# Optimization experiments

Hardware: AMD Instinct MI355X
Metric: run time of the kernel (lower is better)

Reference implementation:

```python
import jax, jax.numpy as jnp
import numpy as np

B, S, D, H, W = 2, 2048, 1024, 16, 256
HD = D // H

def setup_inputs() -> dict:
    key = jax.random.key(0)
    k1, k2, k3 = jax.random.split(key, 3)
    x = jax.random.normal(k1, (B, S, D), dtype=jnp.float32)
    w_qkv = jax.random.normal(k2, (D, 3 * D), dtype=jnp.float32) * (D ** -0.5)
    b_qkv = jnp.zeros((3 * D,), dtype=jnp.float32)
    w_out = jax.random.normal(k3, (D, D), dtype=jnp.float32) * (D ** -0.5)
    b_out = jnp.zeros((D,), dtype=jnp.float32)
    return {"x": x, "w_qkv": w_qkv, "b_qkv": b_qkv, "w_out": w_out, "b_out": b_out}

def reference(x, w_qkv, b_qkv, w_out, b_out):
    b, s, d = x.shape
    qkv = x @ w_qkv + b_qkv                       # [B,S,3D]
    qkv = qkv.reshape(b, s, 3, H, HD)
    q = jnp.transpose(qkv[:, :, 0], (0, 2, 1, 3))  # [B,H,S,HD]
    k = jnp.transpose(qkv[:, :, 1], (0, 2, 1, 3))
    v = jnp.transpose(qkv[:, :, 2], (0, 2, 1, 3))
    # NOTE: original scales by d_model**0.5, not head_dim**0.5
    scores = jnp.einsum('bhqd,bhkd->bhqk', q, k) / (d ** 0.5)
    idx = jnp.arange(s)
    band = jnp.abs(idx[:, None] - idx[None, :]) <= W  # |i-j| <= window_size
    scores = jnp.where(band[None, None], scores, -jnp.inf)
    attn = jax.nn.softmax(scores, axis=-1)
    out = jnp.einsum('bhqk,bhkd->bhqd', attn, v)
    out = jnp.transpose(out, (0, 2, 1, 3)).reshape(b, s, d)
    return out @ w_out + b_out
```

## Files before the change

kernel.cpp:

```cpp
#include <hip/hip_runtime.h>
#include <cstdint>

typedef unsigned short u16;
typedef __attribute__((ext_vector_type(8))) short bf16x8;
typedef __attribute__((ext_vector_type(4))) float f32x4;
typedef __attribute__((ext_vector_type(8))) unsigned short u16x8;

#define DEV static __device__ __forceinline__

DEV u16 f2bf(float f) {
  union { float f; uint32_t u; } v; v.f = f;
  uint32_t r = (v.u + 0x7fffu + ((v.u >> 16) & 1u)) >> 16;
  return (u16)r;
}

DEV void async16(void* lds, const void* g) {
  __builtin_amdgcn_global_load_lds(
      (const __attribute__((address_space(1))) uint32_t*)g,
      (__attribute__((address_space(3))) uint32_t*)lds, 16, 0, 0);
}

__global__ void conv8(const float* __restrict__ in, u16* __restrict__ out, int n8) {
  int i = blockIdx.x * 256 + threadIdx.x;
  if (i >= n8) return;
  const float4* p = (const float4*)in + (size_t)i * 2;
  float4 a = p[0], b = p[1];
  u16x8 ov;
  ov[0] = f2bf(a.x); ov[1] = f2bf(a.y); ov[2] = f2bf(a.z); ov[3] = f2bf(a.w);
  ov[4] = f2bf(b.x); ov[5] = f2bf(b.y); ov[6] = f2bf(b.z); ov[7] = f2bf(b.w);
  *(u16x8*)(out + (size_t)i * 8) = ov;
}

__global__ void tconv(const float* __restrict__ in, u16* __restrict__ out, int R, int Cdim) {
  __shared__ float t[32][33];
  const int tx = threadIdx.x & 31, ty = threadIdx.x >> 5;
  const int r0 = blockIdx.y * 32, c0 = blockIdx.x * 32;
#pragma unroll
  for (int k = 0; k < 4; ++k) {
    int r = ty + k * 8;
    t[r][tx] = in[(size_t)(r0 + r) * Cdim + c0 + tx];
  }
  __syncthreads();
#pragma unroll
  for (int k = 0; k < 4; ++k) {
    int cc = ty + k * 8;
    out[(size_t)(c0 + cc) * R + r0 + tx] = f2bf(t[tx][cc]);
  }
}

template <int EPI>
__global__ __launch_bounds__(256, 2) void gemm_bt(
    const u16* __restrict__ A, const u16* __restrict__ BT,
    const float* __restrict__ bias, float* __restrict__ C,
    u16* __restrict__ qb, u16* __restrict__ kbuf, u16* __restrict__ vtb,
    int Mdim, int Ndim, int Kdim)
{
  __shared__ u16 Alds[128 * 64];
  __shared__ u16 Blds[128 * 64];
  const int tid = threadIdx.x;
  const int wid = tid >> 6, lane = tid & 63;
  const int g = lane >> 4, c = lane & 15;
  const int wr = wid >> 1, wc = wid & 1;
  const int row0 = blockIdx.y * 128, col0 = blockIdx.x * 128;

  f32x4 acc[4][4] = {};

  for (int kt = 0; kt < Kdim; kt += 64) {
    __syncthreads();
#pragma unroll
    for (int it = 0; it < 4; ++it) {
      int chunk = wid * 256 + it * 64 + lane;
      int r = chunk >> 3, j = chunk & 7;
      int js = j ^ (r & 7);
      async16((char*)Alds + (wid * 256 + it * 64) * 16,
              A + (size_t)(row0 + r) * Kdim + kt + js * 8);
      async16((char*)Blds + (wid * 256 + it * 64) * 16,
              BT + (size_t)(col0 + r) * Kdim + kt + js * 8);
    }
    __syncthreads();
#pragma unroll
    for (int kk = 0; kk < 2; ++kk) {
      bf16x8 av[4], bv[4];
#pragma unroll
      for (int mi = 0; mi < 4; ++mi) {
        int r = wr * 64 + mi * 16 + c;
        int js = (kk * 4 + g) ^ (r & 7);
        av[mi] = *(const bf16x8*)((const char*)Alds + r * 128 + js * 16);
      }
#pragma unroll
      for (int ni = 0; ni < 4; ++ni) {
        int r = wc * 64 + ni * 16 + c;
        int js = (kk * 4 + g) ^ (r & 7);
        bv[ni] = *(const bf16x8*)((const char*)Blds + r * 128 + js * 16);
      }
#pragma unroll
      for (int mi = 0; mi < 4; ++mi)
#pragma unroll
        for (int ni = 0; ni < 4; ++ni)
          acc[mi][ni] = __builtin_amdgcn_mfma_f32_16x16x32_bf16(
              av[mi], bv[ni], acc[mi][ni], 0, 0, 0);
    }
  }

#pragma unroll
  for (int mi = 0; mi < 4; ++mi) {
#pragma unroll
    for (int ni = 0; ni < 4; ++ni) {
      int colg = col0 + wc * 64 + ni * 16 + c;
      float bsv = bias[colg];
#pragma unroll
      for (int r = 0; r < 4; ++r) {
        int rowg = row0 + wr * 64 + mi * 16 + g * 4 + r;
        float val = acc[mi][ni][r] + bsv;
        if (EPI == 0) {
          C[(size_t)rowg * Ndim + colg] = val;
        } else {
          int t = colg >> 10, rem = colg & 1023;
          int h = rem >> 6, hd = rem & 63;
          int b = rowg >> 11, s = rowg & 2047;
          size_t bho = (size_t)(b * 16 + h);
          u16 bvv = f2bf(val);
          if (t == 0)      qb  [(bho * 2048 + s) * 64 + hd] = bvv;
          else if (t == 1) kbuf[(bho * 2048 + s) * 64 + hd] = bvv;
          else             vtb [(bho * 64 + hd) * 2048 + s] = bvv;
        }
      }
    }
  }
}

__global__ __launch_bounds__(256, 2) void attn_win(
    const u16* __restrict__ qb, const u16* __restrict__ kb,
    const u16* __restrict__ vtb, u16* __restrict__ hb)
{
  constexpr int S = 2048, W = 256;
  __shared__ u16 Klds[64 * 64];
  __shared__ u16 Vlds[64 * 64];
  __shared__ u16 Plds[4][16 * 64];

  const int tid = threadIdx.x, wid = tid >> 6, lane = tid & 63;
  const int g = lane >> 4, c = lane & 15;
  const int bh = blockIdx.y, qt = blockIdx.x;
  const int q0 = qt * 64;
  const size_t bho = (size_t)bh * S * 64;

  bf16x8 aq[2];
  {
    const u16* qrow = qb + bho + (size_t)(q0 + wid * 16 + c) * 64;
    aq[0] = *(const bf16x8*)(qrow + g * 8);
    aq[1] = *(const bf16x8*)(qrow + 32 + g * 8);
  }
  f32x4 o[4] = {};
  float m[4] = {-1e30f, -1e30f, -1e30f, -1e30f};
  float lsum[4] = {0.f, 0.f, 0.f, 0.f};

  const int kstart = (q0 - W > 0) ? (q0 - W) : 0;
  const int kend = (q0 + 64 + W < S) ? (q0 + 64 + W) : S;
  const float rscale = 0.03125f;

  for (int k0 = kstart; k0 < kend; k0 += 64) {
    __syncthreads();
#pragma unroll
    for (int it = 0; it < 2; ++it) {
      int chunk = wid * 128 + it * 64 + lane;
      int r = chunk >> 3, j = chunk & 7;
      int js = j ^ (r & 7);
      async16((char*)Klds + (wid * 128 + it * 64) * 16,
              kb + bho + (size_t)(k0 + r) * 64 + js * 8);
      async16((char*)Vlds + (wid * 128 + it * 64) * 16,
              vtb + bho + (size_t)r * S + k0 + js * 8);
    }
    __syncthreads();

    f32x4 sacc[4] = {};
#pragma unroll
    for (int kb4 = 0; kb4 < 4; ++kb4) {
      int krow = kb4 * 16 + c;
#pragma unroll
      for (int kk = 0; kk < 2; ++kk) {
        int js = (kk * 4 + g) ^ (krow & 7);
        bf16x8 bk = *(const bf16x8*)((const char*)Klds + krow * 128 + js * 16);
        sacc[kb4] = __builtin_amdgcn_mfma_f32_16x16x32_bf16(aq[kk], bk, sacc[kb4], 0, 0, 0);
      }
    }

    const int qrb = q0 + wid * 16 + g * 4;
    float sc[4][4];
#pragma unroll
    for (int kb4 = 0; kb4 < 4; ++kb4) {
      int key = k0 + kb4 * 16 + c;
#pragma unroll
      for (int r = 0; r < 4; ++r) {
        int d = qrb + r - key;
        bool valid = (d <= W) && (d >= -W);
        sc[kb4][r] = valid ? sacc[kb4][r] * rscale : -1e30f;
      }
    }
    float fscale[4];
#pragma unroll
    for (int r = 0; r < 4; ++r) {
      float mx = fmaxf(fmaxf(sc[0][r], sc[1][r]), fmaxf(sc[2][r], sc[3][r]));
      mx = fmaxf(mx, __shfl_xor(mx, 1));
      mx = fmaxf(mx, __shfl_xor(mx, 2));
      mx = fmaxf(mx, __shfl_xor(mx, 4));
      mx = fmaxf(mx, __shfl_xor(mx, 8));
      float mnew = fmaxf(m[r], mx);
      fscale[r] = __expf(m[r] - mnew);
      m[r] = mnew;
    }
    float rowsum[4] = {0.f, 0.f, 0.f, 0.f};
    u16* Pw = &Plds[wid][0];
#pragma unroll
    for (int kb4 = 0; kb4 < 4; ++kb4) {
#pragma unroll
      for (int r = 0; r < 4; ++r) {
        float p = (sc[kb4][r] > -1e29f) ? __expf(sc[kb4][r] - m[r]) : 0.0f;
        rowsum[r] += p;
        int row = g * 4 + r;
        int key = kb4 * 16 + c;
        int jsw = (key >> 3) ^ (row & 7);
        *((u16*)((char*)Pw + row * 128 + jsw * 16 + (key & 7) * 2)) = f2bf(p);
      }
    }
#pragma unroll
    for (int r = 0; r < 4; ++r) {
      float s2 = rowsum[r];
      s2 += __shfl_xor(s2, 1);
      s2 += __shfl_xor(s2, 2);
      s2 += __shfl_xor(s2, 4);
      s2 += __shfl_xor(s2, 8);
      lsum[r] = lsum[r] * fscale[r] + s2;
      o[0][r] *= fscale[r]; o[1][r] *= fscale[r];
      o[2][r] *= fscale[r]; o[3][r] *= fscale[r];
    }
    asm volatile("s_waitcnt lgkmcnt(0)" ::: "memory");
#pragma unroll
    for (int ks = 0; ks < 2; ++ks) {
      int js = (ks * 4 + g) ^ (c & 7);
      bf16x8 pa = *(const bf16x8*)((const char*)Pw + c * 128 + js * 16);
#pragma unroll
      for (int nb = 0; nb < 4; ++nb) {
        int hd = nb * 16 + c;
        int vjs = (ks * 4 + g) ^ (hd & 7);
        bf16x8 bv = *(const bf16x8*)((const char*)Vlds + hd * 128 + vjs * 16);
        o[nb] = __builtin_amdgcn_mfma_f32_16x16x32_bf16(pa, bv, o[nb], 0, 0, 0);
      }
    }
  }

  const int b = bh >> 4, h = bh & 15;
#pragma unroll
  for (int nb = 0; nb < 4; ++nb) {
#pragma unroll
    for (int r = 0; r < 4; ++r) {
      int qr = q0 + wid * 16 + g * 4 + r;
      int col = h * 64 + nb * 16 + c;
      float val = o[nb][r] / lsum[r];
      hb[(size_t)(b * 2048 + qr) * 1024 + col] = f2bf(val);
    }
  }
}

extern "C" void kernel_launch(void* const* d_in, const int* in_sizes, int n_in,
                              void* d_out, int out_size, void* d_ws, size_t ws_size,
                              hipStream_t stream) {
  const float* x     = (const float*)d_in[0];
  const float* w_qkv = (const float*)d_in[1];
  const float* b_qkv = (const float*)d_in[2];
  const float* w_out = (const float*)d_in[3];
  const float* b_out = (const float*)d_in[4];
  float* out = (float*)d_out;

  char* ws = (char*)d_ws;
  const size_t MB = 1024 * 1024;
  u16* xbf   = (u16*)(ws);
  u16* wqT   = (u16*)(ws + 8 * MB);
  u16* woT   = (u16*)(ws + 14 * MB);
  u16* qbuf  = (u16*)(ws + 16 * MB);
  u16* kbuf  = (u16*)(ws + 24 * MB);
  u16* vtbuf = (u16*)(ws + 32 * MB);
  u16* hbuf  = (u16*)(ws + 40 * MB);

  conv8<<<dim3(4096 * 1024 / 8 / 256), 256, 0, stream>>>(x, xbf, 4096 * 1024 / 8);
  tconv<<<dim3(3072 / 32, 1024 / 32), 256, 0, stream>>>(w_qkv, wqT, 1024, 3072);
  tconv<<<dim3(1024 / 32, 1024 / 32), 256, 0, stream>>>(w_out, woT, 1024, 1024);
  gemm_bt<1><<<dim3(3072 / 128, 4096 / 128), 256, 0, stream>>>(
      xbf, wqT, b_qkv, nullptr, qbuf, kbuf, vtbuf, 4096, 3072, 1024);
  attn_win<<<dim3(2048 / 64, 32), 256, 0, stream>>>(qbuf, kbuf, vtbuf, hbuf);
  gemm_bt<0><<<dim3(1024 / 128, 4096 / 128), 256, 0, stream>>>(
      hbuf, woT, b_out, out, nullptr, nullptr, nullptr, 4096, 1024, 1024);
}
```

Baseline: 179.5 us.

## Restructure windowed attention with double-buffered K/V, larger tiles, lazy rescale

The attention kernel now processes 128 queries per 512-thread block and double-buffers K/V tiles in LDS so the next tile loads while the current one is computed. It skips waves whose rows lie entirely outside the band, skips masking on fully in-band tiles, and folds log2(e) into the scale so it can use exp2. The running max is only rescaled when it grows by more than a threshold. Both GEMM and attention block indices are remapped in an XCD-aware order to improve cache locality. This adds complexity and more LDS per block, and the lazy rescale can change numerics slightly.

```diff
diff --git a/kernel.cpp b/kernel.cpp
--- a/kernel.cpp
+++ b/kernel.cpp
@@ -1,5 +1,6 @@
 #include <hip/hip_runtime.h>
 #include <cstdint>
+#include <cmath>
 
 typedef unsigned short u16;
 typedef __attribute__((ext_vector_type(8))) short bf16x8;
@@ -13,6 +14,8 @@
   uint32_t r = (v.u + 0x7fffu + ((v.u >> 16) & 1u)) >> 16;
   return (u16)r;
 }
+
+DEV float fexp2(float x) { return exp2f(x); }
 
 DEV void async16(void* lds, const void* g) {
   __builtin_amdgcn_global_load_lds(
@@ -61,7 +64,11 @@
   const int wid = tid >> 6, lane = tid & 63;
   const int g = lane >> 4, c = lane & 15;
   const int wr = wid >> 1, wc = wid & 1;
-  const int row0 = blockIdx.y * 128, col0 = blockIdx.x * 128;
+  const int gx = gridDim.x;
+  const int nwg = gx * gridDim.y;
+  const int lin = blockIdx.y * gx + blockIdx.x;
+  const int work = (lin & 7) * (nwg >> 3) + (lin >> 3);
+  const int row0 = (work / gx) * 128, col0 = (work % gx) * 128;
 
   f32x4 acc[4][4] = {};
 
@@ -129,24 +136,27 @@
   }
 }
 
-__global__ __launch_bounds__(256, 2) void attn_win(
+__global__ __launch_bounds__(512, 4) void attn_win(
     const u16* __restrict__ qb, const u16* __restrict__ kb,
     const u16* __restrict__ vtb, u16* __restrict__ hb)
 {
   constexpr int S = 2048, W = 256;
-  __shared__ u16 Klds[64 * 64];
-  __shared__ u16 Vlds[64 * 64];
-  __shared__ u16 Plds[4][16 * 64];
+  __shared__ u16 Klds[2][64 * 64];
+  __shared__ u16 Vlds[2][64 * 64];
+  __shared__ u16 Plds[8][16 * 64];
 
   const int tid = threadIdx.x, wid = tid >> 6, lane = tid & 63;
   const int g = lane >> 4, c = lane & 15;
-  const int bh = blockIdx.y, qt = blockIdx.x;
-  const int q0 = qt * 64;
+  const int lin = blockIdx.x;
+  const int work = (lin & 7) * 64 + (lin >> 3);
+  const int qt = work & 15, bh = work >> 4;
+  const int q0 = qt * 128;
+  const int qr0 = q0 + wid * 16;
   const size_t bho = (size_t)bh * S * 64;
 
   bf16x8 aq[2];
   {
-    const u16* qrow = qb + bho + (size_t)(q0 + wid * 16 + c) * 64;
+    const u16* qrow = qb + bho + (size_t)(qr0 + c) * 64;
     aq[0] = *(const bf16x8*)(qrow + g * 8);
     aq[1] = *(const bf16x8*)(qrow + 32 + g * 8);
   }
@@ -155,108 +165,146 @@
   float lsum[4] = {0.f, 0.f, 0.f, 0.f};
 
   const int kstart = (q0 - W > 0) ? (q0 - W) : 0;
-  const int kend = (q0 + 64 + W < S) ? (q0 + 64 + W) : S;
-  const float rscale = 0.03125f;
-
+  const int kend = (q0 + 128 + W < S) ? (q0 + 128 + W) : S;
+  constexpr float kS = 0.04508422002778011f;
+
+  const int sr = tid >> 3, sj = tid & 7;
+  const int sjs = sj ^ (sr & 7);
+#define STAGE(buf, k0s)                                                         \
+  {                                                                             \
+    async16((char*)&Klds[buf][0] + tid * 16,                                    \
+            kb + bho + (size_t)((k0s) + sr) * 64 + sjs * 8);                    \
+    async16((char*)&Vlds[buf][0] + tid * 16,                                    \
+            vtb + bho + (size_t)sr * S + (k0s) + sjs * 8);                      \
+  }
+
+  STAGE(0, kstart);
+  asm volatile("s_waitcnt vmcnt(0)" ::: "memory");
+  __syncthreads();
+
+  int cur = 0;
   for (int k0 = kstart; k0 < kend; k0 += 64) {
+    if (k0 + 64 < kend) STAGE(cur ^ 1, k0 + 64);
+
+    const bool wave_active = !(k0 > qr0 + 15 + W) && !(k0 + 63 < qr0 - W);
+    if (wave_active) {
+      const u16* Kb = &Klds[cur][0];
+      const u16* Vb = &Vlds[cur][0];
+
+      f32x4 sacc[4] = {};
+#pragma unroll
+      for (int kb4 = 0; kb4 < 4; ++kb4) {
+        int krow = kb4 * 16 + c;
+#pragma unroll
+        for (int kk = 0; kk < 2; ++kk) {
+          int js = (kk * 4 + g) ^ (krow & 7);
+          bf16x8 bk = *(const bf16x8*)((const char*)Kb + krow * 128 + js * 16);
+          sacc[kb4] = __builtin_amdgcn_mfma_f32_16x16x32_bf16(aq[kk], bk, sacc[kb4], 0, 0, 0);
+        }
+      }
+
+      const bool full = (k0 >= qr0 + 15 - W) && (k0 + 63 <= qr0 + W);
+      float sl[4][4];
+      if (full) {
+#pragma unroll
+        for (int kb4 = 0; kb4 < 4; ++kb4)
+#pragma unroll
+          for (int r = 0; r < 4; ++r) sl[kb4][r] = sacc[kb4][r] * kS;
+      } else {
+#pragma unroll
+        for (int kb4 = 0; kb4 < 4; ++kb4) {
+          int key = k0 + kb4 * 16 + c;
+#pragma unroll
+          for (int r = 0; r < 4; ++r) {
+            int d = qr0 + g * 4 + r - key;
+            bool valid = (d <= W) && (d >= -W);
+            sl[kb4][r] = valid ? sacc[kb4][r] * kS : -1e30f;
+          }
+        }
+      }
+
+      float pmax[4];
+#pragma unroll
+      for (int r = 0; r < 4; ++r) {
+        float mx = fmaxf(fmaxf(sl[0][r], sl[1][r]), fmaxf(sl[2][r], sl[3][r]));
+        mx = fmaxf(mx, __shfl_xor(mx, 1));
+        mx = fmaxf(mx, __shfl_xor(mx, 2));
+        mx = fmaxf(mx, __shfl_xor(mx, 4));
+        mx = fmaxf(mx, __shfl_xor(mx, 8));
+        pmax[r] = mx;
+      }
+      float grow = fmaxf(fmaxf(pmax[0] - m[0], pmax[1] - m[1]),
+                         fmaxf(pmax[2] - m[2], pmax[3] - m[3]));
+      if (!__all(grow <= 8.0f)) {
+#pragma unroll
+        for (int r = 0; r < 4; ++r) {
+          float mnew = fmaxf(m[r], pmax[r]);
+          float fs = fexp2(m[r] - mnew);
+          m[r] = mnew;
+          lsum[r] *= fs;
+          o[0][r] *= fs; o[1][r] *= fs; o[2][r] *= fs; o[3][r] *= fs;
+        }
+      }
+
+      float rowsum[4] = {0.f, 0.f, 0.f, 0.f};
+      u16* Pw = &Plds[wid][0];
+#pragma unroll
+      for (int kb4 = 0; kb4 < 4; ++kb4) {
+#pragma unroll
+        for (int r = 0; r < 4; ++r) {
+          float p;
+          if (full) {
+            p = fexp2(sl[kb4][r] - m[r]);
+          } else {
+            p = (sl[kb4][r] > -1e29f) ? fexp2(sl[kb4][r] - m[r]) : 0.0f;
+          }
+          rowsum[r] += p;
+          int row = g * 4 + r;
+          int key = kb4 * 16 + c;
+          int jsw = (key >> 3) ^ (row & 7);
+          *((u16*)((char*)Pw + row * 128 + jsw * 16 + (key & 7) * 2)) = f2bf(p);
+        }
+      }
+#pragma unroll
+      for (int r = 0; r < 4; ++r) {
+        float s2 = rowsum[r];
+        s2 += __shfl_xor(s2, 1);
+        s2 += __shfl_xor(s2, 2);
+        s2 += __shfl_xor(s2, 4);
+        s2 += __shfl_xor(s2, 8);
+        lsum[r] += s2;
+      }
+      asm volatile("s_waitcnt lgkmcnt(0)" ::: "memory");
+      __builtin_amdgcn_sched_barrier(0);
+#pragma unroll
+      for (int ks = 0; ks < 2; ++ks) {
+        int js = (ks * 4 + g) ^ (c & 7);
+        bf16x8 pa = *(const bf16x8*)((const char*)Pw + c * 128 + js * 16);
+#pragma unroll
+        for (int nb = 0; nb < 4; ++nb) {
+          int hd = nb * 16 + c;
+          int vjs = (ks * 4 + g) ^ (hd & 7);
+          bf16x8 bv = *(const bf16x8*)((const char*)Vb + hd * 128 + vjs * 16);
+          o[nb] = __builtin_amdgcn_mfma_f32_16x16x32_bf16(pa, bv, o[nb], 0, 0, 0);
+        }
+      }
+    }
+
+    asm volatile("s_waitcnt vmcnt(0)" ::: "memory");
     __syncthreads();
-#pragma unroll
-    for (int it = 0; it < 2; ++it) {
-      int chunk = wid * 128 + it * 64 + lane;
-      int r = chunk >> 3, j = chunk & 7;
-      int js = j ^ (r & 7);
-      async16((char*)Klds + (wid * 128 + it * 64) * 16,
-              kb + bho + (size_t)(k0 + r) * 64 + js * 8);
-      async16((char*)Vlds + (wid * 128 + it * 64) * 16,
-              vtb + bho + (size_t)r * S + k0 + js * 8);
-    }
-    __syncthreads();
-
-    f32x4 sacc[4] = {};
-#pragma unroll
-    for (int kb4 = 0; kb4 < 4; ++kb4) {
-      int krow = kb4 * 16 + c;
-#pragma unroll
-      for (int kk = 0; kk < 2; ++kk) {
-        int js = (kk * 4 + g) ^ (krow & 7);
-        bf16x8 bk = *(const bf16x8*)((const char*)Klds + krow * 128 + js * 16);
-        sacc[kb4] = __builtin_amdgcn_mfma_f32_16x16x32_bf16(aq[kk], bk, sacc[kb4], 0, 0, 0);
-      }
-    }
-
-    const int qrb = q0 + wid * 16 + g * 4;
-    float sc[4][4];
-#pragma unroll
-    for (int kb4 = 0; kb4 < 4; ++kb4) {
-      int key = k0 + kb4 * 16 + c;
-#pragma unroll
-      for (int r = 0; r < 4; ++r) {
-        int d = qrb + r - key;
-        bool valid = (d <= W) && (d >= -W);
-        sc[kb4][r] = valid ? sacc[kb4][r] * rscale : -1e30f;
-      }
-    }
-    float fscale[4];
-#pragma unroll
-    for (int r = 0; r < 4; ++r) {
-      float mx = fmaxf(fmaxf(sc[0][r], sc[1][r]), fmaxf(sc[2][r], sc[3][r]));
-      mx = fmaxf(mx, __shfl_xor(mx, 1));
-      mx = fmaxf(mx, __shfl_xor(mx, 2));
-      mx = fmaxf(mx, __shfl_xor(mx, 4));
-      mx = fmaxf(mx, __shfl_xor(mx, 8));
-      float mnew = fmaxf(m[r], mx);
-      fscale[r] = __expf(m[r] - mnew);
-      m[r] = mnew;
-    }
-    float rowsum[4] = {0.f, 0.f, 0.f, 0.f};
-    u16* Pw = &Plds[wid][0];
-#pragma unroll
-    for (int kb4 = 0; kb4 < 4; ++kb4) {
-#pragma unroll
-      for (int r = 0; r < 4; ++r) {
-        float p = (sc[kb4][r] > -1e29f) ? __expf(sc[kb4][r] - m[r]) : 0.0f;
-        rowsum[r] += p;
-        int row = g * 4 + r;
-        int key = kb4 * 16 + c;
-        int jsw = (key >> 3) ^ (row & 7);
-        *((u16*)((char*)Pw + row * 128 + jsw * 16 + (key & 7) * 2)) = f2bf(p);
-      }
-    }
-#pragma unroll
-    for (int r = 0; r < 4; ++r) {
-      float s2 = rowsum[r];
-      s2 += __shfl_xor(s2, 1);
-      s2 += __shfl_xor(s2, 2);
-      s2 += __shfl_xor(s2, 4);
-      s2 += __shfl_xor(s2, 8);
-      lsum[r] = lsum[r] * fscale[r] + s2;
-      o[0][r] *= fscale[r]; o[1][r] *= fscale[r];
-      o[2][r] *= fscale[r]; o[3][r] *= fscale[r];
-    }
-    asm volatile("s_waitcnt lgkmcnt(0)" ::: "memory");
-#pragma unroll
-    for (int ks = 0; ks < 2; ++ks) {
-      int js = (ks * 4 + g) ^ (c & 7);
-      bf16x8 pa = *(const bf16x8*)((const char*)Pw + c * 128 + js * 16);
-#pragma unroll
-      for (int nb = 0; nb < 4; ++nb) {
-        int hd = nb * 16 + c;
-        int vjs = (ks * 4 + g) ^ (hd & 7);
-        bf16x8 bv = *(const bf16x8*)((const char*)Vlds + hd * 128 + vjs * 16);
-        o[nb] = __builtin_amdgcn_mfma_f32_16x16x32_bf16(pa, bv, o[nb], 0, 0, 0);
-      }
-    }
-  }
+    cur ^= 1;
+  }
+#undef STAGE
 
   const int b = bh >> 4, h = bh & 15;
 #pragma unroll
-  for (int nb = 0; nb < 4; ++nb) {
-#pragma unroll
-    for (int r = 0; r < 4; ++r) {
-      int qr = q0 + wid * 16 + g * 4 + r;
+  for (int r = 0; r < 4; ++r) {
+    float inv = 1.0f / lsum[r];
+    int qr = qr0 + g * 4 + r;
+#pragma unroll
+    for (int nb = 0; nb < 4; ++nb) {
       int col = h * 64 + nb * 16 + c;
-      float val = o[nb][r] / lsum[r];
-      hb[(size_t)(b * 2048 + qr) * 1024 + col] = f2bf(val);
+      hb[(size_t)(b * 2048 + qr) * 1024 + col] = f2bf(o[nb][r] * inv);
     }
   }
 }
@@ -286,7 +334,7 @@
   tconv<<<dim3(1024 / 32, 1024 / 32), 256, 0, stream>>>(w_out, woT, 1024, 1024);
   gemm_bt<1><<<dim3(3072 / 128, 4096 / 128), 256, 0, stream>>>(
       xbf, wqT, b_qkv, nullptr, qbuf, kbuf, vtbuf, 4096, 3072, 1024);
-  attn_win<<<dim3(2048 / 64, 32), 256, 0, stream>>>(qbuf, kbuf, vtbuf, hbuf);
+  attn_win<<<dim3(512), 512, 0, stream>>>(qbuf, kbuf, vtbuf, hbuf);
   gemm_bt<0><<<dim3(1024 / 128, 4096 / 128), 256, 0, stream>>>(
       hbuf, woT, b_out, out, nullptr, nullptr, nullptr, 4096, 1024, 1024);
 }
```

New measurement: 182.7 us. Within noise of the previous version (+1.7%).
